# Performance work log

Measured on AMD Instinct MI355X. Metric: run time of the kernel, lower is better.

## Reference

```python
import jax, jax.numpy as jnp
import numpy as np

B = 65536
IN1, IN2 = 384, 128
GRU1, GRU2, NLEVELS = 384, 16, 256


def gru_step(x, h, kernel, rkernel, bias):
    """Single Keras GRU (reset_after=True) step. Gate order: z, r, h.
    kernel: [in, 3u], rkernel: [u, 3u], bias: [2, 3u] (input bias, recurrent bias)."""
    u = h.shape[-1]
    xi = x @ kernel + bias[0]          # [B, 3u]
    hr = h @ rkernel + bias[1]         # [B, 3u]
    xz, xr, xh = xi[:, :u], xi[:, u:2 * u], xi[:, 2 * u:]
    hz, hrr, hh = hr[:, :u], hr[:, u:2 * u], hr[:, 2 * u:]
    z = jax.nn.sigmoid(xz + hz)
    r = jax.nn.sigmoid(xr + hrr)
    hcand = jnp.tanh(xh + r * hh)
    return z * h + (1.0 - z) * hcand


def setup_inputs() -> dict:
    key = jax.random.key(0)
    ks = jax.random.split(key, 14)
    s = lambda fan: 1.0 / np.sqrt(fan)
    return {
        "x1": jax.random.normal(ks[0], (B, IN1), jnp.float32),
        "x2": jax.random.normal(ks[1], (B, IN2), jnp.float32),
        "gru1_kernel": jax.random.normal(ks[2], (IN1 + IN2, 3 * GRU1), jnp.float32) * s(IN1 + IN2),
        "gru1_rkernel": jax.random.normal(ks[3], (GRU1, 3 * GRU1), jnp.float32) * s(GRU1),
        "gru1_bias": jax.random.normal(ks[4], (2, 3 * GRU1), jnp.float32) * 0.01,
        "gru2_kernel": jax.random.normal(ks[5], (GRU1, 3 * GRU2), jnp.float32) * s(GRU1),
        "gru2_rkernel": jax.random.normal(ks[6], (GRU2, 3 * GRU2), jnp.float32) * s(GRU2),
        "gru2_bias": jax.random.normal(ks[7], (2, 3 * GRU2), jnp.float32) * 0.01,
        "fc_w1": jax.random.normal(ks[8], (GRU2, NLEVELS), jnp.float32) * s(GRU2),
        "fc_b1": jax.random.normal(ks[9], (NLEVELS,), jnp.float32) * 0.01,
        "fc_w2": jax.random.normal(ks[10], (GRU2, NLEVELS), jnp.float32) * s(GRU2),
        "fc_b2": jax.random.normal(ks[11], (NLEVELS,), jnp.float32) * 0.01,
        "fc_g1": jax.random.normal(ks[12], (NLEVELS,), jnp.float32),
        "fc_g2": jax.random.normal(ks[13], (NLEVELS,), jnp.float32),
    }


def reference(x1, x2, gru1_kernel, gru1_rkernel, gru1_bias,
              gru2_kernel, gru2_rkernel, gru2_bias,
              fc_w1, fc_b1, fc_w2, fc_b2, fc_g1, fc_g2):
    e = jnp.concatenate([x1, x2], axis=-1)                      # [B, 512]
    h1 = gru_step(e, jnp.zeros((e.shape[0], GRU1), e.dtype),
                  gru1_kernel, gru1_rkernel, gru1_bias)         # [B, 384]
    h2 = gru_step(h1, jnp.zeros((e.shape[0], GRU2), e.dtype),
                  gru2_kernel, gru2_rkernel, gru2_bias)         # [B, 16]
    # DualFC (LPCNet): weighted sum of two tanh branches
    d = fc_g1 * jnp.tanh(h2 @ fc_w1 + fc_b1) + fc_g2 * jnp.tanh(h2 @ fc_w2 + fc_b2)
    return jax.nn.softmax(d, axis=-1)                           # [B, 256]
```

## Files before the change

kernel.cpp:

```cpp
#include <hip/hip_runtime.h>

typedef unsigned short u16;
typedef unsigned int   u32;
typedef float f32x4 __attribute__((ext_vector_type(4)));
typedef short s16x8 __attribute__((ext_vector_type(8)));

#define NB    65536
#define K1    512
#define N1    1152
#define G1D   384
#define K2    384
#define N2    48
#define G2D   16
#define NL    256

__device__ inline u16 f2bf(float f) {
  u32 u = __float_as_uint(f);
  u += 0x7fffu + ((u >> 16) & 1u);
  return (u16)(u >> 16);
}
__device__ inline float bf2f(u16 h) { return __uint_as_float(((u32)h) << 16); }
__device__ inline float sigmoidf_(float x) { return 1.0f / (1.0f + __expf(-x)); }
__device__ inline float tanhf_(float x) {
  float e = __expf(2.0f * fabsf(x));
  float t = 1.0f - 2.0f / (e + 1.0f);
  return copysignf(t, x);
}

__device__ inline void gld16(const u16* g, u16* l) {
  __builtin_amdgcn_global_load_lds(
      (const __attribute__((address_space(1))) void*)g,
      (__attribute__((address_space(3))) void*)l, 16, 0, 0);
}

__global__ void prep_a(const float* __restrict__ x1, const float* __restrict__ x2,
                       u16* __restrict__ Abf) {
  int t = blockIdx.x * 256 + threadIdx.x;
  int i = t * 8;
  int row = i >> 9, col = i & 511;
  const float* src = (col < 384) ? (x1 + row * 384 + col) : (x2 + row * 128 + (col - 384));
  float4 v0 = ((const float4*)src)[0];
  float4 v1 = ((const float4*)src)[1];
  union { uint4 v; u16 u[8]; } o;
  o.u[0] = f2bf(v0.x); o.u[1] = f2bf(v0.y); o.u[2] = f2bf(v0.z); o.u[3] = f2bf(v0.w);
  o.u[4] = f2bf(v1.x); o.u[5] = f2bf(v1.y); o.u[6] = f2bf(v1.z); o.u[7] = f2bf(v1.w);
  *(uint4*)(Abf + i) = o.v;
}

__global__ __launch_bounds__(256) void prep_wt1(const float* __restrict__ w,
                                                u16* __restrict__ wt) {
  __shared__ float tile[64][65];
  const int nt = blockIdx.x * 64;
  const int kt = blockIdx.y * 64;
  const int tr = threadIdx.x >> 4;
  const int tc = (threadIdx.x & 15) * 4;
#pragma unroll
  for (int p = 0; p < 4; p++) {
    int k = kt + p * 16 + tr;
    float4 v = *(const float4*)(w + (long)k * N1 + nt + tc);
    tile[p * 16 + tr][tc + 0] = v.x;
    tile[p * 16 + tr][tc + 1] = v.y;
    tile[p * 16 + tr][tc + 2] = v.z;
    tile[p * 16 + tr][tc + 3] = v.w;
  }
  __syncthreads();
  const int nl = threadIdx.x >> 3;
  const int kc = (threadIdx.x & 7) * 8;
#pragma unroll
  for (int p = 0; p < 2; p++) {
    int n = nl + p * 32;
    union { uint4 v; u16 u[8]; } o;
#pragma unroll
    for (int j = 0; j < 8; j++) o.u[j] = f2bf(tile[kc + j][n]);
    *(uint4*)(wt + (long)(nt + n) * K1 + kt + kc) = o.v;
  }
}

__global__ void prep_wt(const float* __restrict__ w, u16* __restrict__ wt, int K, int N) {
  int n = blockIdx.x;
  int k0 = threadIdx.x * 8;
  if (k0 >= K) return;
  union { uint4 v; u16 u[8]; } o;
#pragma unroll
  for (int j = 0; j < 8; j++) o.u[j] = f2bf(w[(k0 + j) * N + n]);
  *(uint4*)(wt + n * K + k0) = o.v;
}

__global__ __launch_bounds__(256) void gemm1gate(const u16* __restrict__ A,
                                                 const u16* __restrict__ Bt,
                                                 const float* __restrict__ bias,
                                                 u16* __restrict__ H1) {
  __shared__ u16 As[128 * 32];
  __shared__ u16 Bs[3][64 * 32];
  const int tid = threadIdx.x;
  const int wave = tid >> 6, lane = tid & 63;
  const int quad = lane >> 4, l16 = lane & 15;
  const int ucbase = blockIdx.x * 64;
  const int mbase = blockIdx.y * 128;
  const int wm = (wave & 1) * 64, wu = (wave >> 1) * 32;

  f32x4 acc[3][4][2];
#pragma unroll
  for (int g = 0; g < 3; g++)
#pragma unroll
    for (int i = 0; i < 4; i++)
#pragma unroll
      for (int j = 0; j < 2; j++)
#pragma unroll
        for (int r = 0; r < 4; r++) acc[g][i][j][r] = 0.0f;

  const int r0 = tid >> 2;
  const int kcg = ((tid & 3) ^ ((r0 >> 1) & 3)) * 8;
  const u16* Aptr = A + (long)(mbase + r0) * K1 + kcg;
  const u16* Bptr0 = Bt + (long)(0 * G1D + ucbase + r0) * K1 + kcg;
  const u16* Bptr1 = Bt + (long)(1 * G1D + ucbase + r0) * K1 + kcg;
  const u16* Bptr2 = Bt + (long)(2 * G1D + ucbase + r0) * K1 + kcg;
  u16* ldsA0 = As + tid * 8;
  u16* ldsA1 = As + 2048 + tid * 8;
  u16* ldsB0 = Bs[0] + tid * 8;
  u16* ldsB1 = Bs[1] + tid * 8;
  u16* ldsB2 = Bs[2] + tid * 8;

  const s16x8* apf[4];
#pragma unroll
  for (int i = 0; i < 4; i++) {
    int ra = wm + i * 16 + l16;
    apf[i] = (const s16x8*)(As + ra * 32 + ((quad ^ ((ra >> 1) & 3)) << 3));
  }
  const s16x8* bpf[3][2];
#pragma unroll
  for (int g = 0; g < 3; g++)
#pragma unroll
    for (int j = 0; j < 2; j++) {
      int rb = wu + j * 16 + l16;
      bpf[g][j] = (const s16x8*)(Bs[g] + rb * 32 + ((quad ^ ((rb >> 1) & 3)) << 3));
    }

  for (int k0 = 0; k0 < K1; k0 += 32) {
    __syncthreads();
    gld16(Aptr + k0, ldsA0);
    gld16(Aptr + 64 * K1 + k0, ldsA1);
    gld16(Bptr0 + k0, ldsB0);
    gld16(Bptr1 + k0, ldsB1);
    gld16(Bptr2 + k0, ldsB2);
    __syncthreads();
    s16x8 af[4];
#pragma unroll
    for (int i = 0; i < 4; i++) af[i] = *apf[i];
#pragma unroll
    for (int g = 0; g < 3; g++) {
      s16x8 bf0 = *bpf[g][0];
      s16x8 bf1 = *bpf[g][1];
#pragma unroll
      for (int mi = 0; mi < 4; mi++) {
        acc[g][mi][0] = __builtin_amdgcn_mfma_f32_16x16x32_bf16(af[mi], bf0, acc[g][mi][0], 0, 0, 0);
        acc[g][mi][1] = __builtin_amdgcn_mfma_f32_16x16x32_bf16(af[mi], bf1, acc[g][mi][1], 0, 0, 0);
      }
    }
  }

#pragma unroll
  for (int j = 0; j < 2; j++) {
    int u = ucbase + wu + j * 16 + l16;
    float bz = bias[u] + bias[1152 + u];
    float br = bias[384 + u] + bias[1536 + u];
    float bh0 = bias[768 + u];
    float bh1 = bias[1920 + u];
#pragma unroll
    for (int mi = 0; mi < 4; mi++) {
#pragma unroll
      for (int rr = 0; rr < 4; rr++) {
        int row = mbase + wm + mi * 16 + quad * 4 + rr;
        float z  = sigmoidf_(acc[0][mi][j][rr] + bz);
        float rg = sigmoidf_(acc[1][mi][j][rr] + br);
        float hc = tanhf_(acc[2][mi][j][rr] + bh0 + rg * bh1);
        H1[(long)row * G1D + u] = f2bf((1.0f - z) * hc);
      }
    }
  }
}

__global__ __launch_bounds__(256) void gemm2(const u16* __restrict__ H1b,
                                             const u16* __restrict__ W2t,
                                             const float* __restrict__ bias2,
                                             float* __restrict__ H2) {
  __shared__ u16 As[128 * 32];
  __shared__ u16 Bs[48 * 32];
  const int tid = threadIdx.x;
  const int wave = tid >> 6, lane = tid & 63;
  const int quad = lane >> 4, l16 = lane & 15;
  const int mbase = blockIdx.x * 128;

  f32x4 acc[2][3];
#pragma unroll
  for (int i = 0; i < 2; i++)
#pragma unroll
    for (int j = 0; j < 3; j++)
#pragma unroll
      for (int r = 0; r < 4; r++) acc[i][j][r] = 0.0f;

  const int r0 = tid >> 2, kc = (tid & 3) * 8;
  const u16* Aptr = H1b + (long)(mbase + r0) * K2 + kc;

  for (int k0 = 0; k0 < K2; k0 += 32) {
    uint4 a0 = *(const uint4*)(Aptr + k0);
    uint4 a1 = *(const uint4*)(Aptr + 64 * K2 + k0);
    uint4 bv;
    if (tid < 192) bv = *(const uint4*)(W2t + r0 * K2 + k0 + kc);
    __syncthreads();
    *(uint4*)(&As[r0 * 32 + kc]) = a0;
    *(uint4*)(&As[(64 + r0) * 32 + kc]) = a1;
    if (tid < 192) *(uint4*)(&Bs[r0 * 32 + kc]) = bv;
    __syncthreads();
    s16x8 af[2], bfr[3];
#pragma unroll
    for (int mi = 0; mi < 2; mi++)
      af[mi] = *(const s16x8*)(&As[(wave * 32 + mi * 16 + l16) * 32 + quad * 8]);
#pragma unroll
    for (int ni = 0; ni < 3; ni++)
      bfr[ni] = *(const s16x8*)(&Bs[(ni * 16 + l16) * 32 + quad * 8]);
#pragma unroll
    for (int mi = 0; mi < 2; mi++)
#pragma unroll
      for (int ni = 0; ni < 3; ni++)
        acc[mi][ni] = __builtin_amdgcn_mfma_f32_16x16x32_bf16(af[mi], bfr[ni], acc[mi][ni], 0, 0, 0);
  }

  const int u = l16;
  const float b0z = bias2[u],      b1z = bias2[48 + u];
  const float b0r = bias2[16 + u], b1r = bias2[64 + u];
  const float b0h = bias2[32 + u], b1h = bias2[80 + u];
#pragma unroll
  for (int mi = 0; mi < 2; mi++) {
#pragma unroll
    for (int rr = 0; rr < 4; rr++) {
      int row = mbase + wave * 32 + mi * 16 + quad * 4 + rr;
      float z  = sigmoidf_(acc[mi][0][rr] + b0z + b1z);
      float rg = sigmoidf_(acc[mi][1][rr] + b0r + b1r);
      float hc = tanhf_(acc[mi][2][rr] + b0h + rg * b1h);
      H2[row * 16 + u] = (1.0f - z) * hc;
    }
  }
}

__global__ __launch_bounds__(256) void fc_softmax(const float* __restrict__ H2,
                                                  const float* __restrict__ w1,
                                                  const float* __restrict__ fb1,
                                                  const float* __restrict__ w2,
                                                  const float* __restrict__ fb2,
                                                  const float* __restrict__ g1,
                                                  const float* __restrict__ g2,
                                                  float* __restrict__ out) {
  int row = blockIdx.x * 4 + (threadIdx.x >> 6);
  int lane = threadIdx.x & 63;
  const float* h2r = H2 + row * 16;
  float h[16];
#pragma unroll
  for (int uu = 0; uu < 16; uu++) h[uu] = h2r[uu];
  float e[4];
  float mx = -1e30f;
#pragma unroll
  for (int i = 0; i < 4; i++) {
    int c = i * 64 + lane;
    float a1 = fb1[c], a2 = fb2[c];
#pragma unroll
    for (int uu = 0; uu < 16; uu++) {
      a1 = fmaf(h[uu], w1[uu * 256 + c], a1);
      a2 = fmaf(h[uu], w2[uu * 256 + c], a2);
    }
    float d = g1[c] * tanhf_(a1) + g2[c] * tanhf_(a2);
    e[i] = d;
    mx = fmaxf(mx, d);
  }
#pragma unroll
  for (int off = 32; off >= 1; off >>= 1) mx = fmaxf(mx, __shfl_xor(mx, off, 64));
  float s = 0.0f;
#pragma unroll
  for (int i = 0; i < 4; i++) { e[i] = __expf(e[i] - mx); s += e[i]; }
#pragma unroll
  for (int off = 32; off >= 1; off >>= 1) s += __shfl_xor(s, off, 64);
  float inv = 1.0f / s;
  float* orow = out + (long)row * 256;
#pragma unroll
  for (int i = 0; i < 4; i++) orow[i * 64 + lane] = e[i] * inv;
}

extern "C" void kernel_launch(void* const* d_in, const int* in_sizes, int n_in,
                              void* d_out, int out_size, void* d_ws, size_t ws_size,
                              hipStream_t stream) {
  const float* x1   = (const float*)d_in[0];
  const float* x2   = (const float*)d_in[1];
  const float* w1k  = (const float*)d_in[2];
  const float* b1g  = (const float*)d_in[4];
  const float* w2k  = (const float*)d_in[5];
  const float* b2g  = (const float*)d_in[7];
  const float* fcw1 = (const float*)d_in[8];
  const float* fcb1 = (const float*)d_in[9];
  const float* fcw2 = (const float*)d_in[10];
  const float* fcb2 = (const float*)d_in[11];
  const float* fcg1 = (const float*)d_in[12];
  const float* fcg2 = (const float*)d_in[13];
  float* out = (float*)d_out;

  char* ws = (char*)d_ws;
  u16* Abf = (u16*)(ws + 0);
  u16* W1t = (u16*)(ws + 67108864);
  u16* H1  = (u16*)(ws + 68288512);
  u16* W2t = (u16*)(ws + 118620160);
  float* H2 = (float*)(ws + 118657024);

  hipLaunchKernelGGL(prep_a, dim3(16384), dim3(256), 0, stream, x1, x2, Abf);
  hipLaunchKernelGGL(prep_wt1, dim3(18, 8), dim3(256), 0, stream, w1k, W1t);
  hipLaunchKernelGGL(prep_wt, dim3(48), dim3(64), 0, stream, w2k, W2t, 384, 48);
  hipLaunchKernelGGL(gemm1gate, dim3(6, 512), dim3(256), 0, stream, Abf, W1t, b1g, H1);
  hipLaunchKernelGGL(gemm2, dim3(512), dim3(256), 0, stream, H1, W2t, b2g, H2);
  hipLaunchKernelGGL(fc_softmax, dim3(16384), dim3(256), 0, stream, H2,
                     fcw1, fcb1, fcw2, fcb2, fcg1, fcg2, out);
}
```

Baseline: 426.6 us.

## Fuse GRU2 and DualFC softmax into one kernel; remap GEMM1 blocks per XCD

Folds the fc_softmax kernel into gemm2. The h2 gate outputs now stay in shared memory instead of making a round trip through global memory, and one launch is removed. Separately, GEMM1 moves to a 1D grid whose block ID mapping gives each XCD a contiguous range of row tiles, so the six column blocks that share an A tile run on the same XCD for L2 reuse. The risk is that fused gemm2fc has only 512 blocks, each looping over 32 rows serially for the softmax, so the output stage has far less parallelism than the old 16384-block kernel.

Measured after the change: 385.2 us. 1.11x faster.

```diff
diff --git a/kernel.cpp b/kernel.cpp
--- a/kernel.cpp
+++ b/kernel.cpp
@@ -10,7 +10,6 @@
 #define N1    1152
 #define G1D   384
 #define K2    384
-#define N2    48
 #define G2D   16
 #define NL    256
 
@@ -95,8 +94,15 @@
   const int tid = threadIdx.x;
   const int wave = tid >> 6, lane = tid & 63;
   const int quad = lane >> 4, l16 = lane & 15;
-  const int ucbase = blockIdx.x * 64;
-  const int mbase = blockIdx.y * 128;
+
+  const int id = blockIdx.x;
+  const int xcd = id & 7;
+  const int s = id >> 3;
+  const int sd6 = s / 6;
+  const int ublk = s - sd6 * 6;
+  const int mbase = (xcd * 64 + sd6) * 128;
+  const int ucbase = ublk * 64;
+
   const int wm = (wave & 1) * 64, wu = (wave >> 1) * 32;
 
   f32x4 acc[3][4][2];
@@ -180,12 +186,19 @@
   }
 }
 
-__global__ __launch_bounds__(256) void gemm2(const u16* __restrict__ H1b,
-                                             const u16* __restrict__ W2t,
-                                             const float* __restrict__ bias2,
-                                             float* __restrict__ H2) {
+__global__ __launch_bounds__(256) void gemm2fc(const u16* __restrict__ H1b,
+                                               const u16* __restrict__ W2t,
+                                               const float* __restrict__ bias2,
+                                               const float* __restrict__ w1,
+                                               const float* __restrict__ fb1,
+                                               const float* __restrict__ w2,
+                                               const float* __restrict__ fb2,
+                                               const float* __restrict__ g1,
+                                               const float* __restrict__ g2,
+                                               float* __restrict__ out) {
   __shared__ u16 As[128 * 32];
   __shared__ u16 Bs[48 * 32];
+  __shared__ float h2s[128 * 17];
   const int tid = threadIdx.x;
   const int wave = tid >> 6, lane = tid & 63;
   const int quad = lane >> 4, l16 = lane & 15;
@@ -226,63 +239,58 @@
         acc[mi][ni] = __builtin_amdgcn_mfma_f32_16x16x32_bf16(af[mi], bfr[ni], acc[mi][ni], 0, 0, 0);
   }
 
-  const int u = l16;
-  const float b0z = bias2[u],      b1z = bias2[48 + u];
-  const float b0r = bias2[16 + u], b1r = bias2[64 + u];
-  const float b0h = bias2[32 + u], b1h = bias2[80 + u];
-#pragma unroll
-  for (int mi = 0; mi < 2; mi++) {
-#pragma unroll
-    for (int rr = 0; rr < 4; rr++) {
-      int row = mbase + wave * 32 + mi * 16 + quad * 4 + rr;
-      float z  = sigmoidf_(acc[mi][0][rr] + b0z + b1z);
-      float rg = sigmoidf_(acc[mi][1][rr] + b0r + b1r);
-      float hc = tanhf_(acc[mi][2][rr] + b0h + rg * b1h);
-      H2[row * 16 + u] = (1.0f - z) * hc;
-    }
-  }
-}
-
-__global__ __launch_bounds__(256) void fc_softmax(const float* __restrict__ H2,
-                                                  const float* __restrict__ w1,
-                                                  const float* __restrict__ fb1,
-                                                  const float* __restrict__ w2,
-                                                  const float* __restrict__ fb2,
-                                                  const float* __restrict__ g1,
-                                                  const float* __restrict__ g2,
-                                                  float* __restrict__ out) {
-  int row = blockIdx.x * 4 + (threadIdx.x >> 6);
-  int lane = threadIdx.x & 63;
-  const float* h2r = H2 + row * 16;
-  float h[16];
-#pragma unroll
-  for (int uu = 0; uu < 16; uu++) h[uu] = h2r[uu];
-  float e[4];
-  float mx = -1e30f;
-#pragma unroll
-  for (int i = 0; i < 4; i++) {
-    int c = i * 64 + lane;
-    float a1 = fb1[c], a2 = fb2[c];
-#pragma unroll
-    for (int uu = 0; uu < 16; uu++) {
-      a1 = fmaf(h[uu], w1[uu * 256 + c], a1);
-      a2 = fmaf(h[uu], w2[uu * 256 + c], a2);
-    }
-    float d = g1[c] * tanhf_(a1) + g2[c] * tanhf_(a2);
-    e[i] = d;
-    mx = fmaxf(mx, d);
-  }
-#pragma unroll
-  for (int off = 32; off >= 1; off >>= 1) mx = fmaxf(mx, __shfl_xor(mx, off, 64));
-  float s = 0.0f;
-#pragma unroll
-  for (int i = 0; i < 4; i++) { e[i] = __expf(e[i] - mx); s += e[i]; }
-#pragma unroll
-  for (int off = 32; off >= 1; off >>= 1) s += __shfl_xor(s, off, 64);
-  float inv = 1.0f / s;
-  float* orow = out + (long)row * 256;
-#pragma unroll
-  for (int i = 0; i < 4; i++) orow[i * 64 + lane] = e[i] * inv;
+  {
+    const int u = l16;
+    const float b0z = bias2[u],      b1z = bias2[48 + u];
+    const float b0r = bias2[16 + u], b1r = bias2[64 + u];
+    const float b0h = bias2[32 + u], b1h = bias2[80 + u];
+#pragma unroll
+    for (int mi = 0; mi < 2; mi++) {
+#pragma unroll
+      for (int rr = 0; rr < 4; rr++) {
+        int row_l = wave * 32 + mi * 16 + quad * 4 + rr;
+        float z  = sigmoidf_(acc[mi][0][rr] + b0z + b1z);
+        float rg = sigmoidf_(acc[mi][1][rr] + b0r + b1r);
+        float hc = tanhf_(acc[mi][2][rr] + b0h + rg * b1h);
+        h2s[row_l * 17 + u] = (1.0f - z) * hc;
+      }
+    }
+  }
+  __syncthreads();
+
+#pragma unroll 1
+  for (int r = 0; r < 32; r++) {
+    int row_l = wave * 32 + r;
+    float h[16];
+#pragma unroll
+    for (int uu = 0; uu < 16; uu++) h[uu] = h2s[row_l * 17 + uu];
+    float e[4];
+    float mx = -1e30f;
+#pragma unroll
+    for (int i = 0; i < 4; i++) {
+      int c = i * 64 + lane;
+      float a1 = fb1[c], a2 = fb2[c];
+#pragma unroll
+      for (int uu = 0; uu < 16; uu++) {
+        a1 = fmaf(h[uu], w1[uu * 256 + c], a1);
+        a2 = fmaf(h[uu], w2[uu * 256 + c], a2);
+      }
+      float d = g1[c] * tanhf_(a1) + g2[c] * tanhf_(a2);
+      e[i] = d;
+      mx = fmaxf(mx, d);
+    }
+#pragma unroll
+    for (int off = 32; off >= 1; off >>= 1) mx = fmaxf(mx, __shfl_xor(mx, off, 64));
+    float sum = 0.0f;
+#pragma unroll
+    for (int i = 0; i < 4; i++) { e[i] = __expf(e[i] - mx); sum += e[i]; }
+#pragma unroll
+    for (int off = 32; off >= 1; off >>= 1) sum += __shfl_xor(sum, off, 64);
+    float inv = 1.0f / sum;
+    float* orow = out + (long)(mbase + row_l) * NL;
+#pragma unroll
+    for (int i = 0; i < 4; i++) orow[i * 64 + lane] = e[i] * inv;
+  }
 }
 
 extern "C" void kernel_launch(void* const* d_in, const int* in_sizes, int n_in,
@@ -307,13 +315,11 @@
   u16* W1t = (u16*)(ws + 67108864);
   u16* H1  = (u16*)(ws + 68288512);
   u16* W2t = (u16*)(ws + 118620160);
-  float* H2 = (float*)(ws + 118657024);
 
   hipLaunchKernelGGL(prep_a, dim3(16384), dim3(256), 0, stream, x1, x2, Abf);
   hipLaunchKernelGGL(prep_wt1, dim3(18, 8), dim3(256), 0, stream, w1k, W1t);
   hipLaunchKernelGGL(prep_wt, dim3(48), dim3(64), 0, stream, w2k, W2t, 384, 48);
-  hipLaunchKernelGGL(gemm1gate, dim3(6, 512), dim3(256), 0, stream, Abf, W1t, b1g, H1);
-  hipLaunchKernelGGL(gemm2, dim3(512), dim3(256), 0, stream, H1, W2t, b2g, H2);
-  hipLaunchKernelGGL(fc_softmax, dim3(16384), dim3(256), 0, stream, H2,
+  hipLaunchKernelGGL(gemm1gate, dim3(3072), dim3(256), 0, stream, Abf, W1t, b1g, H1);
+  hipLaunchKernelGGL(gemm2fc, dim3(512), dim3(256), 0, stream, H1, W2t, b2g,
                      fcw1, fcb1, fcw2, fcb2, fcg1, fcg2, out);
 }
```
